# Performance work log

Measured on AMD Instinct MI355X. Metric: run time of the kernel, lower is better.

The kernel has to match this reference:

```python
import jax, jax.numpy as jnp
import numpy as np

EMBD = 256
HEAD = 4
HD = EMBD // HEAD  # 64
EPS = 1e-5


def setup_inputs() -> dict:
    key = jax.random.key(0)
    ks = jax.random.split(key, 12)
    s = lambda fan_in: 1.0 / np.sqrt(fan_in)
    return {
        "x": jax.random.normal(ks[0], (16, 1024, EMBD), dtype=jnp.float32),
        # attention params (stored as [in, out])
        "qkv_w": jax.random.uniform(ks[1], (EMBD, 3 * EMBD), jnp.float32, -s(EMBD), s(EMBD)),
        "qkv_b": jax.random.uniform(ks[2], (3 * EMBD,), jnp.float32, -s(EMBD), s(EMBD)),
        "out_w": jax.random.uniform(ks[3], (EMBD, EMBD), jnp.float32, -s(EMBD), s(EMBD)),
        "out_b": jax.random.uniform(ks[4], (EMBD,), jnp.float32, -s(EMBD), s(EMBD)),
        # MLP params
        "fc_w": jax.random.uniform(ks[5], (EMBD, 4 * EMBD), jnp.float32, -s(EMBD), s(EMBD)),
        "fc_b": jax.random.uniform(ks[6], (4 * EMBD,), jnp.float32, -s(EMBD), s(EMBD)),
        "proj_w": jax.random.uniform(ks[7], (4 * EMBD, EMBD), jnp.float32, -s(4 * EMBD), s(4 * EMBD)),
        "proj_b": jax.random.uniform(ks[8], (EMBD,), jnp.float32, -s(4 * EMBD), s(4 * EMBD)),
        # LayerNorm params
        "ln1_g": jnp.ones((EMBD,), jnp.float32),
        "ln1_b": jnp.zeros((EMBD,), jnp.float32),
        "ln2_g": jnp.ones((EMBD,), jnp.float32),
        "ln2_b": jnp.zeros((EMBD,), jnp.float32),
    }


def layer_norm(x, g, b):
    mu = jnp.mean(x, axis=-1, keepdims=True)
    var = jnp.mean(jnp.square(x - mu), axis=-1, keepdims=True)
    return (x - mu) * jax.lax.rsqrt(var + EPS) * g + b


def block_forward(x, qkv_w, qkv_b, out_w, out_b, fc_w, fc_b, proj_w, proj_b,
                  ln1_g, ln1_b, ln2_g, ln2_b):
    B, S, E = x.shape
    # --- attention branch ---
    h = layer_norm(x, ln1_g, ln1_b)
    qkv = h @ qkv_w + qkv_b                       # [B,S,3E]
    q, k, v = jnp.split(qkv, 3, axis=-1)
    q = q.reshape(B, S, HEAD, HD).transpose(0, 2, 1, 3)  # [B,H,S,D]
    k = k.reshape(B, S, HEAD, HD).transpose(0, 2, 1, 3)
    v = v.reshape(B, S, HEAD, HD).transpose(0, 2, 1, 3)
    att = jnp.einsum('bhqd,bhkd->bhqk', q, k) / jnp.sqrt(jnp.float32(HD))
    causal = jnp.tril(jnp.ones((S, S), dtype=bool))
    att = jnp.where(causal, att, -jnp.inf)
    att = jax.nn.softmax(att, axis=-1)
    o = jnp.einsum('bhqk,bhkd->bhqd', att, v)     # [B,H,S,D]
    o = o.transpose(0, 2, 1, 3).reshape(B, S, E)
    x = x + o @ out_w + out_b
    # --- MLP branch (dropout inactive at eval) ---
    h = layer_norm(x, ln2_g, ln2_b)
    h = jax.nn.relu(h @ fc_w + fc_b)
    x = x + h @ proj_w + proj_b
    return x


def reference(x, qkv_w, qkv_b, out_w, out_b, fc_w, fc_b, proj_w, proj_b,
              ln1_g, ln1_b, ln2_g, ln2_b):
    return block_forward(x, qkv_w, qkv_b, out_w, out_b, fc_w, fc_b,
                         proj_w, proj_b, ln1_g, ln1_b, ln2_g, ln2_b)
```

## Files before the change

kernel.cpp:

```cpp
#include <hip/hip_runtime.h>
#include <cstdint>


using f32x4 = __attribute__((ext_vector_type(4))) float;
using s16x8 = __attribute__((ext_vector_type(8))) short;
using s16x4 = __attribute__((ext_vector_type(4))) short;

__device__ inline short f2bf(float f) {
    union { float f; unsigned u; } v{f};
    unsigned r = (v.u + 0x7FFFu + ((v.u >> 16) & 1u)) >> 16;
    return (short)r;
}

__device__ inline int cvt_pk_bf16(float lo, float hi) {
    int d;
    asm("v_cvt_pk_bf16_f32 %0, %1, %2" : "=v"(d) : "v"(lo), "v"(hi));
    return d;
}
__device__ inline void swap32(int& a, int& b) {
    asm("v_permlane32_swap_b32 %0, %1" : "+v"(a), "+v"(b));
}
__device__ inline void swap16(int& a, int& b) {
    asm("v_permlane16_swap_b32 %0, %1" : "+v"(a), "+v"(b));
}

__device__ inline void gload16(const void* g, void* l) {
    __builtin_amdgcn_global_load_lds(
        (const __attribute__((address_space(1))) void*)g,
        (__attribute__((address_space(3))) void*)l, 16, 0, 0);
}

__global__ __launch_bounds__(256) void wconv_all_kernel(
    const float* __restrict__ qkv_w, const float* __restrict__ out_w,
    const float* __restrict__ fc_w,  const float* __restrict__ proj_w,
    short* __restrict__ wt_qkv, short* __restrict__ wt_out,
    short* __restrict__ wt_fc,  short* __restrict__ wt_proj)
{
    __shared__ short T[64][65];
    int id = blockIdx.x;
    const float* W; short* Wt; int K, N, nt, kt;
    if (id < 48)       { W = qkv_w;  Wt = wt_qkv;  K = 256;  N = 768;  nt = id % 12;        kt = id / 12; }
    else if (id < 64)  { W = out_w;  Wt = wt_out;  K = 256;  N = 256;  nt = (id - 48) & 3;  kt = (id - 48) >> 2; }
    else if (id < 128) { W = fc_w;   Wt = wt_fc;   K = 256;  N = 1024; nt = (id - 64) & 15; kt = (id - 64) >> 4; }
    else               { W = proj_w; Wt = wt_proj; K = 1024; N = 256;  nt = (id - 128) & 3; kt = (id - 128) >> 2; }
    int n0 = nt * 64, k0 = kt * 64;

    int tid = threadIdx.x;
    int r  = tid >> 2;
    int c  = (tid & 3) << 4;

    const float* src = W + (size_t)(k0 + r) * N + n0 + c;
#pragma unroll
    for (int u = 0; u < 4; ++u) {
        float4 v = *reinterpret_cast<const float4*>(src + u * 4);
        T[r][c + u * 4 + 0] = f2bf(v.x);
        T[r][c + u * 4 + 1] = f2bf(v.y);
        T[r][c + u * 4 + 2] = f2bf(v.z);
        T[r][c + u * 4 + 3] = f2bf(v.w);
    }
    __syncthreads();
    s16x8 o0, o1;
#pragma unroll
    for (int j = 0; j < 8; ++j) { o0[j] = T[c + j][r]; o1[j] = T[c + 8 + j][r]; }
    short* dst = Wt + (size_t)(n0 + r) * K + k0 + c;
    *reinterpret_cast<s16x8*>(dst)     = o0;
    *reinterpret_cast<s16x8*>(dst + 8) = o1;
}

__global__ __launch_bounds__(256) void ln_kernel(const float* __restrict__ x,
                                                 const float* __restrict__ gamma,
                                                 const float* __restrict__ beta,
                                                 short* __restrict__ out)
{
    int tid  = threadIdx.x;
    int lane = tid & 63;
    int row  = blockIdx.x * 4 + (tid >> 6);
    const float* xr = x + (size_t)row * 256;
    float4 v = *reinterpret_cast<const float4*>(xr + lane * 4);

    float s = v.x + v.y + v.z + v.w;
#pragma unroll
    for (int o = 32; o >= 1; o >>= 1) s += __shfl_xor(s, o);
    float mu = s * (1.0f / 256.0f);

    float dx = v.x - mu, dy = v.y - mu, dz = v.z - mu, dw = v.w - mu;
    float q = dx * dx + dy * dy + dz * dz + dw * dw;
#pragma unroll
    for (int o = 32; o >= 1; o >>= 1) q += __shfl_xor(q, o);
    float rstd = rsqrtf(q * (1.0f / 256.0f) + 1e-5f);

    float4 gv = *reinterpret_cast<const float4*>(gamma + lane * 4);
    float4 bv = *reinterpret_cast<const float4*>(beta + lane * 4);
    s16x4 ov;
    ov[0] = f2bf(dx * rstd * gv.x + bv.x);
    ov[1] = f2bf(dy * rstd * gv.y + bv.y);
    ov[2] = f2bf(dz * rstd * gv.z + bv.z);
    ov[3] = f2bf(dw * rstd * gv.w + bv.w);
    *reinterpret_cast<s16x4*>(out + (size_t)row * 256 + lane * 4) = ov;
}

template <int RELU, int RES, int OBF16, int BM, int QKV>
__global__ __launch_bounds__(256) void mgemm_kernel(const short* __restrict__ A,
                                                    const short* __restrict__ Bt,
                                                    const float* __restrict__ bias,
                                                    const float* __restrict__ R,
                                                    void* __restrict__ Cv,
                                                    short* __restrict__ vt,
                                                    int N, int K)
{
    constexpr int MI = BM / 32;
    __shared__ short As[BM * 64];
    __shared__ short Bs[128 * 64];

    int tid = threadIdx.x;
    int l   = tid & 63;
    int w   = tid >> 6;
    int lr  = l & 15;
    int lk8 = (l >> 4) << 3;
    int r4  = (l >> 4) << 2;
    int wr  = w >> 1, wc = w & 1;
    int bn  = blockIdx.x * 128, bm = blockIdx.y * BM;

    int scolS = ((l & 7) << 3) ^ ((l >> 3) << 3);
    int srowA = w * (BM / 4) + (l >> 3);
    int srowB = (w << 5) + (l >> 3);
    const short* pa = A  + (size_t)(bm + srowA) * K + scolS;
    const short* pb = Bt + (size_t)(bn + srowB) * K + scolS;
    short* dstA = As + w * (BM / 4) * 64;
    short* dstB = Bs + (w << 11);

    f32x4 acc[MI][4];
#pragma unroll
    for (int mi = 0; mi < MI; ++mi)
#pragma unroll
        for (int ni = 0; ni < 4; ++ni) acc[mi][ni] = (f32x4){0.f, 0.f, 0.f, 0.f};

    int swz = (lr & 7) << 3;

    for (int k0 = 0; k0 < K; k0 += 64) {
        __syncthreads();
#pragma unroll
        for (int i = 0; i < BM / 32; ++i)
            gload16(pa + (size_t)(i * 8) * K + k0, dstA + (i << 9));
#pragma unroll
        for (int i = 0; i < 4; ++i)
            gload16(pb + (size_t)(i * 8) * K + k0, dstB + (i << 9));
        __syncthreads();

#pragma unroll
        for (int ks = 0; ks < 2; ++ks) {
            s16x8 af[MI], bf[4];
#pragma unroll
            for (int mi = 0; mi < MI; ++mi) {
                int row = wr * (BM / 2) + (mi << 4) + lr;
                af[mi] = *reinterpret_cast<const s16x8*>(
                    &As[(row << 6) + (((ks << 5) + lk8) ^ swz)]);
            }
#pragma unroll
            for (int ni = 0; ni < 4; ++ni) {
                int row = (wc << 6) + (ni << 4) + lr;
                bf[ni] = *reinterpret_cast<const s16x8*>(
                    &Bs[(row << 6) + (((ks << 5) + lk8) ^ swz)]);
            }
#pragma unroll
            for (int mi = 0; mi < MI; ++mi)
#pragma unroll
                for (int ni = 0; ni < 4; ++ni)
                    acc[mi][ni] = __builtin_amdgcn_mfma_f32_16x16x32_bf16(
                        af[mi], bf[ni], acc[mi][ni], 0, 0, 0);
        }
    }

    float bv[4];
#pragma unroll
    for (int ni = 0; ni < 4; ++ni)
        bv[ni] = bias[bn + (wc << 6) + (ni << 4) + lr];

#pragma unroll
    for (int mi = 0; mi < MI; ++mi) {
#pragma unroll
        for (int ni = 0; ni < 4; ++ni) {
            int n = bn + (wc << 6) + (ni << 4) + lr;
#pragma unroll
            for (int r = 0; r < 4; ++r) {
                int m = bm + wr * (BM / 2) + (mi << 4) + r4 + r;
                float v = acc[mi][ni][r] + bv[ni];
                if (RELU) v = fmaxf(v, 0.0f);
                if (RES)  v += R[(size_t)m * N + n];
                if (QKV) {
                    if (bn < 512) {
                        ((short*)Cv)[(size_t)m * 512 + n] = f2bf(v);
                    } else {
                        int hh = (n - 512) >> 6, dd = (n - 512) & 63;
                        int bb = m >> 10, ss = m & 1023;
                        vt[(size_t)((((bb << 2) | hh) << 6) | dd) * 1024 + ss] = f2bf(v);
                    }
                } else if (OBF16) {
                    ((short*)Cv)[(size_t)m * N + n] = f2bf(v);
                } else {
                    ((float*)Cv)[(size_t)m * N + n] = v;
                }
            }
        }
    }
}

__global__ __launch_bounds__(256) void oproj_ln_kernel(const short* __restrict__ A,
                                                       const short* __restrict__ Bt,
                                                       const float* __restrict__ bias,
                                                       const float* __restrict__ R,
                                                       float* __restrict__ x1,
                                                       short* __restrict__ h2,
                                                       const float* __restrict__ g,
                                                       const float* __restrict__ bb)
{
    __shared__ short As[64 * 64];
    __shared__ short Bs[256 * 64];

    int tid = threadIdx.x;
    int l   = tid & 63;
    int w   = tid >> 6;
    int lr  = l & 15;
    int lk8 = (l >> 4) << 3;
    int r4  = (l >> 4) << 2;
    int bm  = blockIdx.x * 64;

    int scolS = ((l & 7) << 3) ^ ((l >> 3) << 3);
    const short* pa = A  + (size_t)(bm + (w << 4) + (l >> 3)) * 256 + scolS;
    const short* pb = Bt + (size_t)((w << 6) + (l >> 3)) * 256 + scolS;
    short* dstA = As + (w << 10);
    short* dstB = Bs + (w << 12);

    f32x4 acc[16];
#pragma unroll
    for (int ni = 0; ni < 16; ++ni) acc[ni] = (f32x4){0.f, 0.f, 0.f, 0.f};

    int swz = (lr & 7) << 3;

    for (int k0 = 0; k0 < 256; k0 += 64) {
        __syncthreads();
#pragma unroll
        for (int i = 0; i < 2; ++i)
            gload16(pa + (size_t)(i * 8) * 256 + k0, dstA + (i << 9));
#pragma unroll
        for (int i = 0; i < 8; ++i)
            gload16(pb + (size_t)(i * 8) * 256 + k0, dstB + (i << 9));
        __syncthreads();

#pragma unroll
        for (int ks = 0; ks < 2; ++ks) {
            int arow = (w << 4) + lr;
            s16x8 af = *reinterpret_cast<const s16x8*>(
                &As[(arow << 6) + (((ks << 5) + lk8) ^ swz)]);
#pragma unroll
            for (int ni = 0; ni < 16; ++ni) {
                int row = (ni << 4) + lr;
                s16x8 bf = *reinterpret_cast<const s16x8*>(
                    &Bs[(row << 6) + (((ks << 5) + lk8) ^ swz)]);
                acc[ni] = __builtin_amdgcn_mfma_f32_16x16x32_bf16(af, bf, acc[ni], 0, 0, 0);
            }
        }
    }

#pragma unroll
    for (int ni = 0; ni < 16; ++ni) {
        int n = (ni << 4) + lr;
        float bvx = bias[n];
#pragma unroll
        for (int r = 0; r < 4; ++r) {
            int m = bm + (w << 4) + r4 + r;
            acc[ni][r] += bvx + R[(size_t)m * 256 + n];
        }
    }
#pragma unroll
    for (int r = 0; r < 4; ++r) {
        float s = 0.0f;
#pragma unroll
        for (int ni = 0; ni < 16; ++ni) s += acc[ni][r];
        s += __shfl_xor(s, 1); s += __shfl_xor(s, 2);
        s += __shfl_xor(s, 4); s += __shfl_xor(s, 8);
        float mu = s * (1.0f / 256.0f);
        float q = 0.0f;
#pragma unroll
        for (int ni = 0; ni < 16; ++ni) {
            float d = acc[ni][r] - mu;
            q += d * d;
        }
        q += __shfl_xor(q, 1); q += __shfl_xor(q, 2);
        q += __shfl_xor(q, 4); q += __shfl_xor(q, 8);
        float rstd = rsqrtf(q * (1.0f / 256.0f) + 1e-5f);

        int m = bm + (w << 4) + r4 + r;
#pragma unroll
        for (int ni = 0; ni < 16; ++ni) {
            int n = (ni << 4) + lr;
            float v = acc[ni][r];
            x1[(size_t)m * 256 + n] = v;
            h2[(size_t)m * 256 + n] = f2bf((v - mu) * rstd * g[n] + bb[n]);
        }
    }
}

__global__ __launch_bounds__(256, 2) void attn_kernel(const short* __restrict__ qk,
                                                      const short* __restrict__ vt,
                                                      short* __restrict__ o)
{
    __shared__ short Ks[2][64 * 64];
    __shared__ short Vs[2][64 * 64];

    int bid  = blockIdx.x;
    int xcd  = bid & 7;
    int pair = (bid >> 3) & 7;
    int bhg  = bid >> 6;
    int bh   = (bhg << 3) | xcd;
    int b = bh >> 2, h = bh & 3;

    int tid = threadIdx.x;
    int l   = tid & 63;
    int w   = tid >> 6;
    int lr  = l & 15;
    int g   = l >> 4;
    int lk8 = g << 3;
    int w16 = w << 4;

    int srow = (w << 3) + (l >> 3);
    int scol = ((l & 7) << 3) ^ (((l >> 3) & 7) << 3);
    const short* kgp = qk + (size_t)(b * 1024 + srow) * 512 + 256 + h * 64 + scol;
    const short* vgp = vt + (size_t)((bh << 6) + srow) * 1024 + scol;
    short* dstK = &Ks[0][(w << 3) * 64];
    short* dstV = &Vs[0][(w << 3) * 64];
    const int BUFS = 64 * 64;

    const float SC = 0.125f * 1.44269504088896f;
    int rsw = (lr & 7) << 3;

    int cur = 1;
    for (int sel = 0; sel < 2; ++sel) {
        int qt = sel == 0 ? pair : 15 - pair;

        const short* qrow = qk + (size_t)(b * 1024 + qt * 64 + w16 + lr) * 512 + h * 64;
        s16x8 qf[2];
        qf[0] = *reinterpret_cast<const s16x8*>(qrow + lk8);
        qf[1] = *reinterpret_cast<const s16x8*>(qrow + 32 + lk8);

#pragma unroll
        for (int i = 0; i < 2; ++i) {
            gload16(kgp + (size_t)(qt * 0 + i * 32) * 512, dstK + (cur ^ 1) * BUFS + (i << 11));
            gload16(vgp + (size_t)(i * 32) * 1024,         dstV + (cur ^ 1) * BUFS + (i << 11));
        }
        __syncthreads();
        cur ^= 1;

        float m = -1e30f, lsum = 0.0f;
        f32x4 oacc[4];
#pragma unroll
        for (int dt = 0; dt < 4; ++dt) oacc[dt] = (f32x4){0.f, 0.f, 0.f, 0.f};
        int qglob = qt * 64 + w16 + lr;

        for (int kt = 0; kt <= qt; ++kt) {
            if (kt < qt) {
#pragma unroll
                for (int i = 0; i < 2; ++i) {
                    gload16(kgp + (size_t)((kt + 1) * 64 + i * 32) * 512,
                            dstK + (cur ^ 1) * BUFS + (i << 11));
                    gload16(vgp + (size_t)(i * 32) * 1024 + (kt + 1) * 64,
                            dstV + (cur ^ 1) * BUFS + (i << 11));
                }
            }

            f32x4 s[4];
#pragma unroll
            for (int jt = 0; jt < 4; ++jt) s[jt] = (f32x4){0.f, 0.f, 0.f, 0.f};
#pragma unroll
            for (int ks = 0; ks < 2; ++ks) {
#pragma unroll
                for (int jt = 0; jt < 4; ++jt) {
                    int row = jt * 16 + lr;
                    s16x8 kf = *reinterpret_cast<const s16x8*>(
                        &Ks[cur][(row << 6) + ((32 * ks + lk8) ^ rsw)]);
                    s[jt] = __builtin_amdgcn_mfma_f32_16x16x32_bf16(kf, qf[ks], s[jt], 0, 0, 0);
                }
            }
#pragma unroll
            for (int jt = 0; jt < 4; ++jt)
#pragma unroll
                for (int r = 0; r < 4; ++r) s[jt][r] *= SC;

            if (kt == qt) {
#pragma unroll
                for (int jt = 0; jt < 4; ++jt) {
                    int kb = kt * 64 + jt * 16 + (g << 2);
#pragma unroll
                    for (int r = 0; r < 4; ++r)
                        if (kb + r > qglob) s[jt][r] = -1e30f;
                }
            }

            float rm = fmaxf(fmaxf(s[0][0], s[0][1]), fmaxf(s[0][2], s[0][3]));
#pragma unroll
            for (int jt = 1; jt < 4; ++jt)
                rm = fmaxf(rm, fmaxf(fmaxf(s[jt][0], s[jt][1]), fmaxf(s[jt][2], s[jt][3])));
            rm = fmaxf(rm, __shfl_xor(rm, 16));
            rm = fmaxf(rm, __shfl_xor(rm, 32));
            float mn  = fmaxf(m, rm);
            float fct = exp2f(m - mn);
            m = mn;
            float ps = 0.0f;
#pragma unroll
            for (int jt = 0; jt < 4; ++jt)
#pragma unroll
                for (int r = 0; r < 4; ++r) {
                    float p = exp2f(s[jt][r] - mn);
                    s[jt][r] = p;
                    ps += p;
                }
            ps += __shfl_xor(ps, 16);
            ps += __shfl_xor(ps, 32);
            lsum = lsum * fct + ps;

            int cpk[4][2];
#pragma unroll
            for (int jt = 0; jt < 4; ++jt) {
                cpk[jt][0] = cvt_pk_bf16(s[jt][0], s[jt][1]);
                cpk[jt][1] = cvt_pk_bf16(s[jt][2], s[jt][3]);
            }

#pragma unroll
            for (int r = 0; r < 4; ++r) {
                float f4 = __shfl(fct, 4 * g + r);
#pragma unroll
                for (int dt = 0; dt < 4; ++dt) oacc[dt][r] *= f4;
            }

#pragma unroll
            for (int ks = 0; ks < 2; ++ks) {
                int a0 = cpk[2 * ks][0],     a1 = cpk[2 * ks][1];
                int b0 = cpk[2 * ks + 1][0], b1 = cpk[2 * ks + 1][1];
                swap32(a0, b0); swap32(a1, b1);
                swap16(a0, b0); swap16(a1, b1);
                union { int i[4]; s16x8 v; } fr;
                fr.i[0] = a0; fr.i[1] = a1; fr.i[2] = b0; fr.i[3] = b1;
#pragma unroll
                for (int dt = 0; dt < 4; ++dt) {
                    int row = dt * 16 + lr;
                    s16x8 vf = *reinterpret_cast<const s16x8*>(
                        &Vs[cur][(row << 6) + ((32 * ks + lk8) ^ rsw)]);
                    oacc[dt] = __builtin_amdgcn_mfma_f32_16x16x32_bf16(fr.v, vf, oacc[dt], 0, 0, 0);
                }
            }

            if (kt < qt) {
                __syncthreads();
                cur ^= 1;
            }
        }

#pragma unroll
        for (int r = 0; r < 4; ++r) {
            float lv  = __shfl(lsum, 4 * g + r);
            float inv = 1.0f / lv;
            short* orow = o + (size_t)(b * 1024 + qt * 64 + w16 + 4 * g + r) * 256 + h * 64;
#pragma unroll
            for (int dt = 0; dt < 4; ++dt)
                orow[dt * 16 + lr] = f2bf(oacc[dt][r] * inv);
        }
    }
}

extern "C" void kernel_launch(void* const* d_in, const int* in_sizes, int n_in,
                              void* d_out, int out_size, void* d_ws, size_t ws_size,
                              hipStream_t stream)
{
    const float* x      = (const float*)d_in[0];
    const float* qkv_w  = (const float*)d_in[1];
    const float* qkv_b  = (const float*)d_in[2];
    const float* out_w  = (const float*)d_in[3];
    const float* out_b  = (const float*)d_in[4];
    const float* fc_w   = (const float*)d_in[5];
    const float* fc_b   = (const float*)d_in[6];
    const float* proj_w = (const float*)d_in[7];
    const float* proj_b = (const float*)d_in[8];
    const float* ln1_g  = (const float*)d_in[9];
    const float* ln1_b  = (const float*)d_in[10];
    const float* ln2_g  = (const float*)d_in[11];
    const float* ln2_b  = (const float*)d_in[12];
    float* out = (float*)d_out;

    short* ws = (short*)d_ws;
    short* wt_qkv  = ws;
    short* wt_out  = ws + 196608;
    short* wt_fc   = ws + 262144;
    short* wt_proj = ws + 524288;
    short* bufA    = ws + 786432;
    short* qk_buf  = ws + 4980736;
    short* vt_buf  = ws + 13369344;
    short* h3_buf  = ws + 4980736;

    dim3 blk(256);

    wconv_all_kernel<<<dim3(192), blk, 0, stream>>>(
        qkv_w, out_w, fc_w, proj_w, wt_qkv, wt_out, wt_fc, wt_proj);
    ln_kernel<<<dim3(4096), blk, 0, stream>>>(x, ln1_g, ln1_b, bufA);
    mgemm_kernel<0, 0, 1, 128, 1><<<dim3(6, 128), blk, 0, stream>>>(
        bufA, wt_qkv, qkv_b, nullptr, qk_buf, vt_buf, 768, 256);
    attn_kernel<<<dim3(512), blk, 0, stream>>>(qk_buf, vt_buf, bufA);
    oproj_ln_kernel<<<dim3(256), blk, 0, stream>>>(
        bufA, wt_out, out_b, x, out, bufA, ln2_g, ln2_b);
    mgemm_kernel<1, 0, 1, 128, 0><<<dim3(8, 128), blk, 0, stream>>>(
        bufA, wt_fc, fc_b, nullptr, h3_buf, nullptr, 1024, 256);
    mgemm_kernel<0, 1, 0, 64, 0><<<dim3(2, 256), blk, 0, stream>>>(
        h3_buf, wt_proj, proj_b, out, out, nullptr, 256, 1024);
}
```

Baseline: 125.4 us.

## Double-buffer GEMM tiles, split attention per query tile, add lazy rescale

The GEMM and out-proj+LN kernels now double-buffer their shared-memory tiles, prefetching the next K slice while computing on the current one, and raise wave priority around MFMA bursts. The attention kernel now gives each block a single query tile instead of a balanced pair, launches twice as many blocks, and raises occupancy bounds to 4. Its online softmax skips the rescale unless the running max grows by more than a threshold. These changes aim to hide global-load latency and improve occupancy and balance, at the cost of doubled LDS use in the GEMMs and possibly uneven work across attention blocks.

After: 132.3 us. 1.06x slower.

```diff
diff --git a/kernel.cpp b/kernel.cpp
--- a/kernel.cpp
+++ b/kernel.cpp
@@ -108,9 +108,11 @@
                                                     short* __restrict__ vt,
                                                     int N, int K)
 {
-    constexpr int MI = BM / 32;
-    __shared__ short As[BM * 64];
-    __shared__ short Bs[128 * 64];
+    constexpr int MI  = BM / 32;
+    constexpr int ASZ = BM * 64;
+    constexpr int BSZ = 128 * 64;
+    __shared__ short As[2 * ASZ];
+    __shared__ short Bs[2 * BSZ];
 
     int tid = threadIdx.x;
     int l   = tid & 63;
@@ -137,16 +139,27 @@
 
     int swz = (lr & 7) << 3;
 
+#pragma unroll
+    for (int i = 0; i < BM / 32; ++i)
+        gload16(pa + (size_t)(i * 8) * K, dstA + (i << 9));
+#pragma unroll
+    for (int i = 0; i < 4; ++i)
+        gload16(pb + (size_t)(i * 8) * K, dstB + (i << 9));
+    __syncthreads();
+
+    int cur = 0;
     for (int k0 = 0; k0 < K; k0 += 64) {
-        __syncthreads();
-#pragma unroll
-        for (int i = 0; i < BM / 32; ++i)
-            gload16(pa + (size_t)(i * 8) * K + k0, dstA + (i << 9));
-#pragma unroll
-        for (int i = 0; i < 4; ++i)
-            gload16(pb + (size_t)(i * 8) * K + k0, dstB + (i << 9));
-        __syncthreads();
-
+        if (k0 + 64 < K) {
+            int nxt = cur ^ 1;
+#pragma unroll
+            for (int i = 0; i < BM / 32; ++i)
+                gload16(pa + (size_t)(i * 8) * K + k0 + 64, dstA + nxt * ASZ + (i << 9));
+#pragma unroll
+            for (int i = 0; i < 4; ++i)
+                gload16(pb + (size_t)(i * 8) * K + k0 + 64, dstB + nxt * BSZ + (i << 9));
+        }
+        const short* curA = As + cur * ASZ;
+        const short* curB = Bs + cur * BSZ;
 #pragma unroll
         for (int ks = 0; ks < 2; ++ks) {
             s16x8 af[MI], bf[4];
@@ -154,21 +167,25 @@
             for (int mi = 0; mi < MI; ++mi) {
                 int row = wr * (BM / 2) + (mi << 4) + lr;
                 af[mi] = *reinterpret_cast<const s16x8*>(
-                    &As[(row << 6) + (((ks << 5) + lk8) ^ swz)]);
+                    &curA[(row << 6) + (((ks << 5) + lk8) ^ swz)]);
             }
 #pragma unroll
             for (int ni = 0; ni < 4; ++ni) {
                 int row = (wc << 6) + (ni << 4) + lr;
                 bf[ni] = *reinterpret_cast<const s16x8*>(
-                    &Bs[(row << 6) + (((ks << 5) + lk8) ^ swz)]);
-            }
+                    &curB[(row << 6) + (((ks << 5) + lk8) ^ swz)]);
+            }
+            __builtin_amdgcn_s_setprio(1);
 #pragma unroll
             for (int mi = 0; mi < MI; ++mi)
 #pragma unroll
                 for (int ni = 0; ni < 4; ++ni)
                     acc[mi][ni] = __builtin_amdgcn_mfma_f32_16x16x32_bf16(
                         af[mi], bf[ni], acc[mi][ni], 0, 0, 0);
-        }
+            __builtin_amdgcn_s_setprio(0);
+        }
+        __syncthreads();
+        cur ^= 1;
     }
 
     float bv[4];
@@ -214,8 +231,10 @@
                                                        const float* __restrict__ g,
                                                        const float* __restrict__ bb)
 {
-    __shared__ short As[64 * 64];
-    __shared__ short Bs[256 * 64];
+    constexpr int ASZ = 64 * 64;
+    constexpr int BSZ = 256 * 64;
+    __shared__ short As[2 * ASZ];
+    __shared__ short Bs[2 * BSZ];
 
     int tid = threadIdx.x;
     int l   = tid & 63;
@@ -237,29 +256,44 @@
 
     int swz = (lr & 7) << 3;
 
+#pragma unroll
+    for (int i = 0; i < 2; ++i)
+        gload16(pa + (size_t)(i * 8) * 256, dstA + (i << 9));
+#pragma unroll
+    for (int i = 0; i < 8; ++i)
+        gload16(pb + (size_t)(i * 8) * 256, dstB + (i << 9));
+    __syncthreads();
+
+    int cur = 0;
     for (int k0 = 0; k0 < 256; k0 += 64) {
-        __syncthreads();
-#pragma unroll
-        for (int i = 0; i < 2; ++i)
-            gload16(pa + (size_t)(i * 8) * 256 + k0, dstA + (i << 9));
-#pragma unroll
-        for (int i = 0; i < 8; ++i)
-            gload16(pb + (size_t)(i * 8) * 256 + k0, dstB + (i << 9));
-        __syncthreads();
-
+        if (k0 + 64 < 256) {
+            int nxt = cur ^ 1;
+#pragma unroll
+            for (int i = 0; i < 2; ++i)
+                gload16(pa + (size_t)(i * 8) * 256 + k0 + 64, dstA + nxt * ASZ + (i << 9));
+#pragma unroll
+            for (int i = 0; i < 8; ++i)
+                gload16(pb + (size_t)(i * 8) * 256 + k0 + 64, dstB + nxt * BSZ + (i << 9));
+        }
+        const short* curA = As + cur * ASZ;
+        const short* curB = Bs + cur * BSZ;
 #pragma unroll
         for (int ks = 0; ks < 2; ++ks) {
             int arow = (w << 4) + lr;
             s16x8 af = *reinterpret_cast<const s16x8*>(
-                &As[(arow << 6) + (((ks << 5) + lk8) ^ swz)]);
+                &curA[(arow << 6) + (((ks << 5) + lk8) ^ swz)]);
+            __builtin_amdgcn_s_setprio(1);
 #pragma unroll
             for (int ni = 0; ni < 16; ++ni) {
                 int row = (ni << 4) + lr;
                 s16x8 bf = *reinterpret_cast<const s16x8*>(
-                    &Bs[(row << 6) + (((ks << 5) + lk8) ^ swz)]);
+                    &curB[(row << 6) + (((ks << 5) + lk8) ^ swz)]);
                 acc[ni] = __builtin_amdgcn_mfma_f32_16x16x32_bf16(af, bf, acc[ni], 0, 0, 0);
             }
-        }
+            __builtin_amdgcn_s_setprio(0);
+        }
+        __syncthreads();
+        cur ^= 1;
     }
 
 #pragma unroll
@@ -301,7 +335,7 @@
     }
 }
 
-__global__ __launch_bounds__(256, 2) void attn_kernel(const short* __restrict__ qk,
+__global__ __launch_bounds__(256, 4) void attn_kernel(const short* __restrict__ qk,
                                                       const short* __restrict__ vt,
                                                       short* __restrict__ o)
 {
@@ -310,8 +344,11 @@
 
     int bid  = blockIdx.x;
     int xcd  = bid & 7;
-    int pair = (bid >> 3) & 7;
-    int bhg  = bid >> 6;
+    int rest = bid >> 3;
+    int tq   = rest & 15;
+    int flip = (rest >> 5) & 1;
+    int qt   = flip ? 15 - tq : tq;
+    int bhg  = rest >> 4;
     int bh   = (bhg << 3) | xcd;
     int b = bh >> 2, h = bh & 3;
 
@@ -334,136 +371,142 @@
     const float SC = 0.125f * 1.44269504088896f;
     int rsw = (lr & 7) << 3;
 
-    int cur = 1;
-    for (int sel = 0; sel < 2; ++sel) {
-        int qt = sel == 0 ? pair : 15 - pair;
-
-        const short* qrow = qk + (size_t)(b * 1024 + qt * 64 + w16 + lr) * 512 + h * 64;
-        s16x8 qf[2];
-        qf[0] = *reinterpret_cast<const s16x8*>(qrow + lk8);
-        qf[1] = *reinterpret_cast<const s16x8*>(qrow + 32 + lk8);
-
-#pragma unroll
-        for (int i = 0; i < 2; ++i) {
-            gload16(kgp + (size_t)(qt * 0 + i * 32) * 512, dstK + (cur ^ 1) * BUFS + (i << 11));
-            gload16(vgp + (size_t)(i * 32) * 1024,         dstV + (cur ^ 1) * BUFS + (i << 11));
-        }
-        __syncthreads();
-        cur ^= 1;
-
-        float m = -1e30f, lsum = 0.0f;
-        f32x4 oacc[4];
-#pragma unroll
-        for (int dt = 0; dt < 4; ++dt) oacc[dt] = (f32x4){0.f, 0.f, 0.f, 0.f};
-        int qglob = qt * 64 + w16 + lr;
-
-        for (int kt = 0; kt <= qt; ++kt) {
-            if (kt < qt) {
-#pragma unroll
-                for (int i = 0; i < 2; ++i) {
-                    gload16(kgp + (size_t)((kt + 1) * 64 + i * 32) * 512,
-                            dstK + (cur ^ 1) * BUFS + (i << 11));
-                    gload16(vgp + (size_t)(i * 32) * 1024 + (kt + 1) * 64,
-                            dstV + (cur ^ 1) * BUFS + (i << 11));
-                }
-            }
-
-            f32x4 s[4];
-#pragma unroll
-            for (int jt = 0; jt < 4; ++jt) s[jt] = (f32x4){0.f, 0.f, 0.f, 0.f};
-#pragma unroll
-            for (int ks = 0; ks < 2; ++ks) {
-#pragma unroll
-                for (int jt = 0; jt < 4; ++jt) {
-                    int row = jt * 16 + lr;
-                    s16x8 kf = *reinterpret_cast<const s16x8*>(
-                        &Ks[cur][(row << 6) + ((32 * ks + lk8) ^ rsw)]);
-                    s[jt] = __builtin_amdgcn_mfma_f32_16x16x32_bf16(kf, qf[ks], s[jt], 0, 0, 0);
-                }
-            }
-#pragma unroll
-            for (int jt = 0; jt < 4; ++jt)
-#pragma unroll
-                for (int r = 0; r < 4; ++r) s[jt][r] *= SC;
-
-            if (kt == qt) {
-#pragma unroll
-                for (int jt = 0; jt < 4; ++jt) {
-                    int kb = kt * 64 + jt * 16 + (g << 2);
-#pragma unroll
-                    for (int r = 0; r < 4; ++r)
-                        if (kb + r > qglob) s[jt][r] = -1e30f;
-                }
-            }
-
-            float rm = fmaxf(fmaxf(s[0][0], s[0][1]), fmaxf(s[0][2], s[0][3]));
-#pragma unroll
-            for (int jt = 1; jt < 4; ++jt)
-                rm = fmaxf(rm, fmaxf(fmaxf(s[jt][0], s[jt][1]), fmaxf(s[jt][2], s[jt][3])));
-            rm = fmaxf(rm, __shfl_xor(rm, 16));
-            rm = fmaxf(rm, __shfl_xor(rm, 32));
-            float mn  = fmaxf(m, rm);
-            float fct = exp2f(m - mn);
+    const short* qrow = qk + (size_t)(b * 1024 + qt * 64 + w16 + lr) * 512 + h * 64;
+    s16x8 qf[2];
+    qf[0] = *reinterpret_cast<const s16x8*>(qrow + lk8);
+    qf[1] = *reinterpret_cast<const s16x8*>(qrow + 32 + lk8);
+
+#pragma unroll
+    for (int i = 0; i < 2; ++i) {
+        gload16(kgp + (size_t)(i * 32) * 512, dstK + (i << 11));
+        gload16(vgp + (size_t)(i * 32) * 1024, dstV + (i << 11));
+    }
+    __syncthreads();
+
+    float m = -1e30f, lsum = 0.0f;
+    f32x4 oacc[4];
+#pragma unroll
+    for (int dt = 0; dt < 4; ++dt) oacc[dt] = (f32x4){0.f, 0.f, 0.f, 0.f};
+    int qglob = qt * 64 + w16 + lr;
+    int cur = 0;
+
+    for (int kt = 0; kt <= qt; ++kt) {
+        if (kt < qt) {
+            int nxt = cur ^ 1;
+#pragma unroll
+            for (int i = 0; i < 2; ++i) {
+                gload16(kgp + (size_t)((kt + 1) * 64 + i * 32) * 512,
+                        dstK + nxt * BUFS + (i << 11));
+                gload16(vgp + (size_t)(i * 32) * 1024 + (kt + 1) * 64,
+                        dstV + nxt * BUFS + (i << 11));
+            }
+        }
+
+        f32x4 s[4];
+#pragma unroll
+        for (int jt = 0; jt < 4; ++jt) s[jt] = (f32x4){0.f, 0.f, 0.f, 0.f};
+        __builtin_amdgcn_s_setprio(1);
+#pragma unroll
+        for (int ks = 0; ks < 2; ++ks) {
+#pragma unroll
+            for (int jt = 0; jt < 4; ++jt) {
+                int row = jt * 16 + lr;
+                s16x8 kf = *reinterpret_cast<const s16x8*>(
+                    &Ks[cur][(row << 6) + ((32 * ks + lk8) ^ rsw)]);
+                s[jt] = __builtin_amdgcn_mfma_f32_16x16x32_bf16(kf, qf[ks], s[jt], 0, 0, 0);
+            }
+        }
+        __builtin_amdgcn_s_setprio(0);
+#pragma unroll
+        for (int jt = 0; jt < 4; ++jt)
+#pragma unroll
+            for (int r = 0; r < 4; ++r) s[jt][r] *= SC;
+
+        if (kt == qt) {
+#pragma unroll
+            for (int jt = 0; jt < 4; ++jt) {
+                int kb = kt * 64 + jt * 16 + (g << 2);
+#pragma unroll
+                for (int r = 0; r < 4; ++r)
+                    if (kb + r > qglob) s[jt][r] = -1e30f;
+            }
+        }
+
+        float rm = fmaxf(fmaxf(s[0][0], s[0][1]), fmaxf(s[0][2], s[0][3]));
+#pragma unroll
+        for (int jt = 1; jt < 4; ++jt)
+            rm = fmaxf(rm, fmaxf(fmaxf(s[jt][0], s[jt][1]), fmaxf(s[jt][2], s[jt][3])));
+        rm = fmaxf(rm, __shfl_xor(rm, 16));
+        rm = fmaxf(rm, __shfl_xor(rm, 32));
+        bool big = __any(rm > m + 8.0f);
+        float fct = 1.0f;
+        if (big) {
+            float mn = fmaxf(m, rm);
+            fct = exp2f(m - mn);
             m = mn;
-            float ps = 0.0f;
-#pragma unroll
-            for (int jt = 0; jt < 4; ++jt)
-#pragma unroll
-                for (int r = 0; r < 4; ++r) {
-                    float p = exp2f(s[jt][r] - mn);
-                    s[jt][r] = p;
-                    ps += p;
-                }
-            ps += __shfl_xor(ps, 16);
-            ps += __shfl_xor(ps, 32);
-            lsum = lsum * fct + ps;
-
-            int cpk[4][2];
-#pragma unroll
-            for (int jt = 0; jt < 4; ++jt) {
-                cpk[jt][0] = cvt_pk_bf16(s[jt][0], s[jt][1]);
-                cpk[jt][1] = cvt_pk_bf16(s[jt][2], s[jt][3]);
-            }
-
+        }
+        float ps = 0.0f;
+#pragma unroll
+        for (int jt = 0; jt < 4; ++jt)
+#pragma unroll
+            for (int r = 0; r < 4; ++r) {
+                float p = exp2f(s[jt][r] - m);
+                s[jt][r] = p;
+                ps += p;
+            }
+        ps += __shfl_xor(ps, 16);
+        ps += __shfl_xor(ps, 32);
+        lsum = lsum * fct + ps;
+
+        int cpk[4][2];
+#pragma unroll
+        for (int jt = 0; jt < 4; ++jt) {
+            cpk[jt][0] = cvt_pk_bf16(s[jt][0], s[jt][1]);
+            cpk[jt][1] = cvt_pk_bf16(s[jt][2], s[jt][3]);
+        }
+
+        if (big) {
 #pragma unroll
             for (int r = 0; r < 4; ++r) {
                 float f4 = __shfl(fct, 4 * g + r);
 #pragma unroll
                 for (int dt = 0; dt < 4; ++dt) oacc[dt][r] *= f4;
             }
-
-#pragma unroll
-            for (int ks = 0; ks < 2; ++ks) {
-                int a0 = cpk[2 * ks][0],     a1 = cpk[2 * ks][1];
-                int b0 = cpk[2 * ks + 1][0], b1 = cpk[2 * ks + 1][1];
-                swap32(a0, b0); swap32(a1, b1);
-                swap16(a0, b0); swap16(a1, b1);
-                union { int i[4]; s16x8 v; } fr;
-                fr.i[0] = a0; fr.i[1] = a1; fr.i[2] = b0; fr.i[3] = b1;
-#pragma unroll
-                for (int dt = 0; dt < 4; ++dt) {
-                    int row = dt * 16 + lr;
-                    s16x8 vf = *reinterpret_cast<const s16x8*>(
-                        &Vs[cur][(row << 6) + ((32 * ks + lk8) ^ rsw)]);
-                    oacc[dt] = __builtin_amdgcn_mfma_f32_16x16x32_bf16(fr.v, vf, oacc[dt], 0, 0, 0);
-                }
-            }
-
-            if (kt < qt) {
-                __syncthreads();
-                cur ^= 1;
-            }
-        }
-
-#pragma unroll
-        for (int r = 0; r < 4; ++r) {
-            float lv  = __shfl(lsum, 4 * g + r);
-            float inv = 1.0f / lv;
-            short* orow = o + (size_t)(b * 1024 + qt * 64 + w16 + 4 * g + r) * 256 + h * 64;
-#pragma unroll
-            for (int dt = 0; dt < 4; ++dt)
-                orow[dt * 16 + lr] = f2bf(oacc[dt][r] * inv);
-        }
+        }
+
+#pragma unroll
+        for (int ks = 0; ks < 2; ++ks) {
+            int a0 = cpk[2 * ks][0],     a1 = cpk[2 * ks][1];
+            int b0 = cpk[2 * ks + 1][0], b1 = cpk[2 * ks + 1][1];
+            swap32(a0, b0); swap32(a1, b1);
+            swap16(a0, b0); swap16(a1, b1);
+            union { int i[4]; s16x8 v; } fr;
+            fr.i[0] = a0; fr.i[1] = a1; fr.i[2] = b0; fr.i[3] = b1;
+            __builtin_amdgcn_s_setprio(1);
+#pragma unroll
+            for (int dt = 0; dt < 4; ++dt) {
+                int row = dt * 16 + lr;
+                s16x8 vf = *reinterpret_cast<const s16x8*>(
+                    &Vs[cur][(row << 6) + ((32 * ks + lk8) ^ rsw)]);
+                oacc[dt] = __builtin_amdgcn_mfma_f32_16x16x32_bf16(fr.v, vf, oacc[dt], 0, 0, 0);
+            }
+            __builtin_amdgcn_s_setprio(0);
+        }
+
+        if (kt < qt) {
+            __syncthreads();
+            cur ^= 1;
+        }
+    }
+
+#pragma unroll
+    for (int r = 0; r < 4; ++r) {
+        float lv  = __shfl(lsum, 4 * g + r);
+        float inv = 1.0f / lv;
+        short* orow = o + (size_t)(b * 1024 + qt * 64 + w16 + 4 * g + r) * 256 + h * 64;
+#pragma unroll
+        for (int dt = 0; dt < 4; ++dt)
+            orow[dt * 16 + lr] = f2bf(oacc[dt][r] * inv);
     }
 }
 
@@ -503,7 +546,7 @@
     ln_kernel<<<dim3(4096), blk, 0, stream>>>(x, ln1_g, ln1_b, bufA);
     mgemm_kernel<0, 0, 1, 128, 1><<<dim3(6, 128), blk, 0, stream>>>(
         bufA, wt_qkv, qkv_b, nullptr, qk_buf, vt_buf, 768, 256);
-    attn_kernel<<<dim3(512), blk, 0, stream>>>(qk_buf, vt_buf, bufA);
+    attn_kernel<<<dim3(1024), blk, 0, stream>>>(qk_buf, vt_buf, bufA);
     oproj_ln_kernel<<<dim3(256), blk, 0, stream>>>(
         bufA, wt_out, out_b, x, out, bufA, ln2_g, ln2_b);
     mgemm_kernel<1, 0, 1, 128, 0><<<dim3(8, 128), blk, 0, stream>>>(
```
